# Kernel optimization log

Measured on AMD Instinct MI355X. Metric: run time of the kernel, lower is better.

The kernel has to match this reference:

```python
import jax, jax.numpy as jnp
import numpy as np

N_NODES = 100000
N_EDGES = 1600000
N_GRAPHS = 64
D_IN, D_HID, D_LAT = 2, 64, 32


def setup_inputs() -> dict:
    key = jax.random.key(0)
    k1, k2, k3, k4, k5, k6, k7 = jax.random.split(key, 7)
    x = jax.random.normal(k1, (N_NODES, D_IN), dtype=jnp.float32)
    edge_index = jax.random.randint(k2, (2, N_EDGES), 0, N_NODES, dtype=jnp.int64)
    batch = jnp.sort(jax.random.randint(k3, (N_NODES,), 0, N_GRAPHS, dtype=jnp.int64))
    # GCNConv params (glorot-ish scale)
    W1 = jax.random.normal(k4, (D_IN, D_HID), dtype=jnp.float32) * (1.0 / np.sqrt(D_IN))
    b1 = jnp.zeros((D_HID,), dtype=jnp.float32)
    W2 = jax.random.normal(k5, (D_HID, D_LAT), dtype=jnp.float32) * (1.0 / np.sqrt(D_HID))
    b2 = jnp.zeros((D_LAT,), dtype=jnp.float32)
    return {"x": x, "W1": W1, "b1": b1, "W2": W2, "b2": b2,
            "edge_index": edge_index, "batch": batch}


def _gcn_conv(x, W, b, src, dst, n_nodes):
    """PyG GCNConv: add self-loops, symmetric deg^-1/2 normalization, linear, scatter-add."""
    h = x @ W  # [N, d_out]
    loop = jnp.arange(n_nodes, dtype=src.dtype)
    src_f = jnp.concatenate([src, loop])
    dst_f = jnp.concatenate([dst, loop])
    deg = jax.ops.segment_sum(jnp.ones_like(dst_f, dtype=h.dtype), dst_f,
                              num_segments=n_nodes)  # in-degree incl. self-loop
    dis = jnp.where(deg > 0, jax.lax.rsqrt(deg), 0.0)
    norm = dis[src_f] * dis[dst_f]  # [E+N]
    msg = h[src_f] * norm[:, None]  # edge gather (memory-bound)
    out = jax.ops.segment_sum(msg, dst_f, num_segments=n_nodes)
    return out + b


def reference(x, W1, b1, W2, b2, edge_index, batch):
    src, dst = edge_index[0], edge_index[1]
    n = x.shape[0]
    h = jax.nn.relu(_gcn_conv(x, W1, b1, src, dst, n))
    z = _gcn_conv(h, W2, b2, src, dst, n)
    # global_mean_pool over graph ids
    sums = jax.ops.segment_sum(z, batch, num_segments=N_GRAPHS)
    cnts = jax.ops.segment_sum(jnp.ones((n,), dtype=z.dtype), batch,
                               num_segments=N_GRAPHS)
    return sums / jnp.maximum(cnts, 1.0)[:, None]
```

## Files before the change

kernel.cpp:

```cpp
#include <hip/hip_runtime.h>
#include <hip/hip_fp16.h>

#define N_NODES  100000
#define N_EDGES  1600000
#define N_GRAPHS 64
#define NBUCK    391
#define NBLK     256
#define CHUNK    (N_EDGES / NBLK)
#define NODEBLK  1563

#define OFF_GSTART 0
#define OFF_ROWPTR 128
#define OFF_DIS    100224
#define OFF_S      200320
#define OFF_CSR    400384
#define OFF_Q      2000384
#define OFF_BHIST  2000384
#define OFF_BOFFL  2100736
#define OFF_BSUM   2201088
#define OFF_BSTART 2201600
#define OFF_TMP    2202112

typedef float fvec2 __attribute__((ext_vector_type(2)));

__device__ __forceinline__ int excl_scan_256(int v, int* wsum) {
  int t = threadIdx.x, lane = t & 63, w = t >> 6;
  int x = v;
#pragma unroll
  for (int off = 1; off < 64; off <<= 1) {
    int y = __shfl_up(x, off, 64);
    if (lane >= off) x += y;
  }
  if (lane == 63) wsum[w] = x;
  __syncthreads();
  if (t == 0) {
    int r = 0;
#pragma unroll
    for (int i = 0; i < 4; ++i) { int tv = wsum[i]; wsum[i] = r; r += tv; }
  }
  __syncthreads();
  return x - v + wsum[w];
}

__device__ __forceinline__ int excl_scan_512(int v, int* wsum) {
  int t = threadIdx.x, lane = t & 63, w = t >> 6;
  int x = v;
#pragma unroll
  for (int off = 1; off < 64; off <<= 1) {
    int y = __shfl_up(x, off, 64);
    if (lane >= off) x += y;
  }
  if (lane == 63) wsum[w] = x;
  __syncthreads();
  if (t == 0) {
    int r = 0;
#pragma unroll
    for (int i = 0; i < 8; ++i) { int tv = wsum[i]; wsum[i] = r; r += tv; }
  }
  __syncthreads();
  return x - v + wsum[w];
}

__global__ void k_hist(const int* __restrict__ dst, int* __restrict__ bhist) {
  __shared__ int hist[NBUCK];
  int t = threadIdx.x, k = blockIdx.x;
  for (int b = t; b < NBUCK; b += 256) hist[b] = 0;
  __syncthreads();
  int e0 = k * CHUNK, e1 = e0 + CHUNK;
  for (int e = e0 + t; e < e1; e += 256) atomicAdd(&hist[dst[e] >> 8], 1);
  __syncthreads();
  for (int b = t; b < NBUCK; b += 256) bhist[b * NBLK + k] = hist[b];
}

__global__ void k_scan_a(const int* __restrict__ bhist, int* __restrict__ boffl,
                         int* __restrict__ bsum, const int* __restrict__ batch,
                         int* __restrict__ gstart) {
  __shared__ int wsum[4];
  int t = threadIdx.x, b = blockIdx.x;
  int i = b * 256 + t;
  if (i < N_NODES) {
    int bi = batch[i];
    if (i == 0) {
      for (int g = 0; g <= bi; ++g) gstart[g] = 0;
    } else {
      int bp = batch[i - 1];
      for (int g = bp + 1; g <= bi; ++g) gstart[g] = i;
    }
    if (i == N_NODES - 1) {
      for (int g = bi + 1; g <= N_GRAPHS; ++g) gstart[g] = N_NODES;
    }
  }
  int v = bhist[b * NBLK + t];
  int ex = excl_scan_256(v, wsum);
  boffl[b * NBLK + t] = ex;
  if (t == NBLK - 1) bsum[b] = ex + v;
}

__global__ void k_scan_b(const int* __restrict__ bsum, int* __restrict__ bstart,
                         float* __restrict__ pooled) {
  __shared__ int wsum[8];
  int t = threadIdx.x;
  for (int i = t; i < N_GRAPHS * 32; i += 512) pooled[i] = 0.f;
  int v = (t < NBUCK) ? bsum[t] : 0;
  int ex = excl_scan_512(v, wsum);
  if (t <= NBUCK) bstart[t] = ex;
}

__global__ void k_scatter(const int* __restrict__ src, const int* __restrict__ dst,
                          const int* __restrict__ bstart, const int* __restrict__ boffl,
                          int* __restrict__ tmp) {
  __shared__ int sbase[NBUCK];
  __shared__ int fill[NBUCK];
  int t = threadIdx.x, k = blockIdx.x;
  for (int b = t; b < NBUCK; b += 256) {
    sbase[b] = bstart[b] + boffl[b * NBLK + k];
    fill[b] = 0;
  }
  __syncthreads();
  int e0 = k * CHUNK, e1 = e0 + CHUNK;
  for (int e = e0 + t; e < e1; e += 256) {
    int s_ = src[e], d_ = dst[e];
    int b = d_ >> 8;
    int pos = sbase[b] + atomicAdd(&fill[b], 1);
    tmp[pos] = (s_ << 8) | (d_ & 255);
  }
}

__global__ void k_fine(const int* __restrict__ tmp, const int* __restrict__ bstart,
                       const float* __restrict__ x, int* __restrict__ csr_src,
                       int* __restrict__ row_ptr, float* __restrict__ dis,
                       float2* __restrict__ s) {
  __shared__ int hist[256];
  __shared__ int fill[256];
  __shared__ int wsum[4];
  int t = threadIdx.x, b = blockIdx.x;
  int base_n = b << 8;
  int e0 = bstart[b], e1 = bstart[b + 1];
  hist[t] = 0;
  __syncthreads();
  for (int e = e0 + t; e < e1; e += 256) atomicAdd(&hist[tmp[e] & 255], 1);
  __syncthreads();
  int h = hist[t];
  int ex = excl_scan_256(h, wsum);
  hist[t] = ex;
  fill[t] = 0;
  int nn = min(256, N_NODES - base_n);
  if (t < nn) {
    int v = base_n + t;
    row_ptr[v] = e0 + ex;
    float dv = rsqrtf((float)(h + 1));
    dis[v] = dv;
    float2 xv = ((const float2*)x)[v];
    s[v] = make_float2(xv.x * dv, xv.y * dv);
  }
  if (b == NBUCK - 1 && t == 0) row_ptr[N_NODES] = e1;
  __syncthreads();
  for (int e = e0 + t; e < e1; e += 256) {
    int p = tmp[e];
    int fine = p & 255;
    int pos = e0 + hist[fine] + atomicAdd(&fill[fine], 1);
    csr_src[pos] = p >> 8;
  }
}

__global__ void k_layer1(const float2* __restrict__ s, const float* __restrict__ dis,
                         const int* __restrict__ row_ptr, const int* __restrict__ csr_src,
                         const float* __restrict__ W1, const float* __restrict__ b1,
                         const float* __restrict__ W2, int4* __restrict__ q8) {
  __shared__ float4 sWB[64];
  __shared__ float4 sW2[512];
  int tid = threadIdx.x;
  if (tid < 64) sWB[tid] = make_float4(W1[tid], W1[64 + tid], b1[tid], 0.f);
  for (int i = tid; i < 512; i += 256) sW2[i] = ((const float4*)W2)[i];
  __syncthreads();
  int v = blockIdx.x * 256 + tid;
  if (v >= N_NODES) return;
  int beg = row_ptr[v], end = row_ptr[v + 1];
  float2 sv = s[v];
  float t0 = sv.x, t1 = sv.y;
  int k = beg;
  for (; k + 4 <= end; k += 4) {
    int u0 = csr_src[k], u1 = csr_src[k + 1], u2 = csr_src[k + 2], u3 = csr_src[k + 3];
    float2 a = s[u0], b = s[u1], c = s[u2], d = s[u3];
    t0 += (a.x + b.x) + (c.x + d.x);
    t1 += (a.y + b.y) + (c.y + d.y);
  }
  for (; k < end; ++k) {
    float2 su = s[csr_src[k]];
    t0 += su.x;
    t1 += su.y;
  }
  float dv = dis[v];
  t0 *= dv;
  t1 *= dv;
  float4 a4[8];
#pragma unroll
  for (int m = 0; m < 8; ++m) a4[m] = make_float4(0.f, 0.f, 0.f, 0.f);
  for (int j = 0; j < 64; ++j) {
    float4 wb = sWB[j];
    float r = fmaxf(fmaf(t0, wb.x, fmaf(t1, wb.y, wb.z)), 0.f);
#pragma unroll
    for (int m = 0; m < 8; ++m) {
      float4 w = sW2[j * 8 + m];
      a4[m].x = fmaf(r, w.x, a4[m].x);
      a4[m].y = fmaf(r, w.y, a4[m].y);
      a4[m].z = fmaf(r, w.z, a4[m].z);
      a4[m].w = fmaf(r, w.w, a4[m].w);
    }
  }
  int pk[8];
#pragma unroll
  for (int m = 0; m < 8; ++m) {
    int wrd = __builtin_amdgcn_cvt_pk_fp8_f32(a4[m].x * dv, a4[m].y * dv, 0, false);
    wrd = __builtin_amdgcn_cvt_pk_fp8_f32(a4[m].z * dv, a4[m].w * dv, wrd, true);
    pk[m] = wrd;
  }
  q8[v * 2]     = make_int4(pk[0], pk[1], pk[2], pk[3]);
  q8[v * 2 + 1] = make_int4(pk[4], pk[5], pk[6], pk[7]);
}

__device__ __forceinline__ float4 qdec(unsigned int d) {
  fvec2 lo = __builtin_amdgcn_cvt_pk_f32_fp8(d, false);
  fvec2 hi = __builtin_amdgcn_cvt_pk_f32_fp8(d, true);
  return make_float4(lo.x, lo.y, hi.x, hi.y);
}

__global__ void k_layer2(const unsigned int* __restrict__ q, const float* __restrict__ dis,
                         const int* __restrict__ row_ptr, const int* __restrict__ csr_src,
                         const int* __restrict__ batch, float* __restrict__ pooled) {
  __shared__ float4 red[32][9];
  int t = threadIdx.x;
  int fp = t & 7;
  int rg = t >> 3;
  int vb = blockIdx.x * 64;
  int nlast = min(vb + 63, N_NODES - 1);
  bool uniform = (batch[vb] == batch[nlast]);
  int v0 = vb + rg * 2;
  int v1 = min(v0 + 2, N_NODES);
  float4 acc = make_float4(0.f, 0.f, 0.f, 0.f);
  int curg = (v0 < N_NODES) ? batch[v0] : -1;
  for (int v = v0; v < v1; ++v) {
    if (!uniform) {
      int g = batch[v];
      if (g != curg) {
        int base = curg * 32 + fp * 4;
        atomicAdd(&pooled[base],     acc.x);
        atomicAdd(&pooled[base + 1], acc.y);
        atomicAdd(&pooled[base + 2], acc.z);
        atomicAdd(&pooled[base + 3], acc.w);
        acc = make_float4(0.f, 0.f, 0.f, 0.f);
        curg = g;
      }
    }
    int e0 = row_ptr[v], e1 = row_ptr[v + 1];
    float4 z = qdec(q[v * 8 + fp]);
    int k = e0;
    for (; k + 8 <= e1; k += 8) {
      int u0 = csr_src[k],     u1 = csr_src[k + 1], u2 = csr_src[k + 2], u3 = csr_src[k + 3];
      int u4 = csr_src[k + 4], u5 = csr_src[k + 5], u6 = csr_src[k + 6], u7 = csr_src[k + 7];
      float4 f0 = qdec(q[u0 * 8 + fp]);
      float4 f1 = qdec(q[u1 * 8 + fp]);
      float4 f2 = qdec(q[u2 * 8 + fp]);
      float4 f3 = qdec(q[u3 * 8 + fp]);
      float4 f4 = qdec(q[u4 * 8 + fp]);
      float4 f5 = qdec(q[u5 * 8 + fp]);
      float4 f6 = qdec(q[u6 * 8 + fp]);
      float4 f7 = qdec(q[u7 * 8 + fp]);
      z.x += ((f0.x + f1.x) + (f2.x + f3.x)) + ((f4.x + f5.x) + (f6.x + f7.x));
      z.y += ((f0.y + f1.y) + (f2.y + f3.y)) + ((f4.y + f5.y) + (f6.y + f7.y));
      z.z += ((f0.z + f1.z) + (f2.z + f3.z)) + ((f4.z + f5.z) + (f6.z + f7.z));
      z.w += ((f0.w + f1.w) + (f2.w + f3.w)) + ((f4.w + f5.w) + (f6.w + f7.w));
    }
    for (; k < e1; ++k) {
      float4 f = qdec(q[csr_src[k] * 8 + fp]);
      z.x += f.x; z.y += f.y; z.z += f.z; z.w += f.w;
    }
    float dvv = dis[v];
    acc.x = fmaf(z.x, dvv, acc.x);
    acc.y = fmaf(z.y, dvv, acc.y);
    acc.z = fmaf(z.z, dvv, acc.z);
    acc.w = fmaf(z.w, dvv, acc.w);
  }
  if (uniform) {
    red[rg][fp] = acc;
    __syncthreads();
    if (t < 8) {
      float4 ssum = make_float4(0.f, 0.f, 0.f, 0.f);
#pragma unroll
      for (int r = 0; r < 32; ++r) {
        float4 x4 = red[r][t];
        ssum.x += x4.x; ssum.y += x4.y; ssum.z += x4.z; ssum.w += x4.w;
      }
      int gg = batch[vb];
      int base = gg * 32 + t * 4;
      atomicAdd(&pooled[base],     ssum.x);
      atomicAdd(&pooled[base + 1], ssum.y);
      atomicAdd(&pooled[base + 2], ssum.z);
      atomicAdd(&pooled[base + 3], ssum.w);
    }
  } else if (v0 < N_NODES) {
    int base = curg * 32 + fp * 4;
    atomicAdd(&pooled[base],     acc.x);
    atomicAdd(&pooled[base + 1], acc.y);
    atomicAdd(&pooled[base + 2], acc.z);
    atomicAdd(&pooled[base + 3], acc.w);
  }
}

__global__ void k_final(float* __restrict__ out, const int* __restrict__ gstart,
                        const float* __restrict__ b2) {
  int i = blockIdx.x * 256 + threadIdx.x;
  if (i < N_GRAPHS * 32) {
    int g = i >> 5, l = i & 31;
    int c = gstart[g + 1] - gstart[g];
    out[i] = (c > 0) ? out[i] / (float)c + b2[l] : 0.f;
  }
}

extern "C" void kernel_launch(void* const* d_in, const int* in_sizes, int n_in,
                              void* d_out, int out_size, void* d_ws, size_t ws_size,
                              hipStream_t stream) {
  (void)in_sizes; (void)n_in; (void)out_size; (void)ws_size;
  const float* x   = (const float*)d_in[0];
  const float* W1  = (const float*)d_in[1];
  const float* b1  = (const float*)d_in[2];
  const float* W2  = (const float*)d_in[3];
  const float* b2  = (const float*)d_in[4];
  const int* edge  = (const int*)d_in[5];
  const int* batch = (const int*)d_in[6];
  const int* src = edge;
  const int* dst = edge + N_EDGES;
  float* out = (float*)d_out;

  int* ws      = (int*)d_ws;
  int* gstart  = ws + OFF_GSTART;
  int* row_ptr = ws + OFF_ROWPTR;
  float* dis   = (float*)(ws + OFF_DIS);
  float2* s    = (float2*)(ws + OFF_S);
  int* csr_src = ws + OFF_CSR;
  int4* q8     = (int4*)(ws + OFF_Q);
  int* bhist   = ws + OFF_BHIST;
  int* boffl   = ws + OFF_BOFFL;
  int* bsum    = ws + OFF_BSUM;
  int* bstart  = ws + OFF_BSTART;
  int* tmp     = ws + OFF_TMP;

  k_hist<<<NBLK, 256, 0, stream>>>(dst, bhist);
  k_scan_a<<<NBUCK, 256, 0, stream>>>(bhist, boffl, bsum, batch, gstart);
  k_scan_b<<<1, 512, 0, stream>>>(bsum, bstart, out);
  k_scatter<<<NBLK, 256, 0, stream>>>(src, dst, bstart, boffl, tmp);
  k_fine<<<NBUCK, 256, 0, stream>>>(tmp, bstart, x, csr_src, row_ptr, dis, s);
  k_layer1<<<(N_NODES + 255) / 256, 256, 0, stream>>>(s, dis, row_ptr, csr_src,
                                                      W1, b1, W2, q8);
  k_layer2<<<NODEBLK, 256, 0, stream>>>((const unsigned int*)q8, dis, row_ptr,
                                        csr_src, batch, out);
  k_final<<<8, 256, 0, stream>>>(out, gstart, b2);
}
```

Before: 97.16 us.

## Fuse scan and finalize kernels via last-block pattern; rework layer1 to two nodes per thread

```diff
diff --git a/kernel.cpp b/kernel.cpp
--- a/kernel.cpp
+++ b/kernel.cpp
@@ -10,6 +10,7 @@
 #define NODEBLK  1563
 
 #define OFF_GSTART 0
+#define OFF_CNT    80
 #define OFF_ROWPTR 128
 #define OFF_DIS    100224
 #define OFF_S      200320
@@ -42,28 +43,11 @@
   return x - v + wsum[w];
 }
 
-__device__ __forceinline__ int excl_scan_512(int v, int* wsum) {
-  int t = threadIdx.x, lane = t & 63, w = t >> 6;
-  int x = v;
-#pragma unroll
-  for (int off = 1; off < 64; off <<= 1) {
-    int y = __shfl_up(x, off, 64);
-    if (lane >= off) x += y;
-  }
-  if (lane == 63) wsum[w] = x;
-  __syncthreads();
-  if (t == 0) {
-    int r = 0;
-#pragma unroll
-    for (int i = 0; i < 8; ++i) { int tv = wsum[i]; wsum[i] = r; r += tv; }
-  }
-  __syncthreads();
-  return x - v + wsum[w];
-}
-
-__global__ void k_hist(const int* __restrict__ dst, int* __restrict__ bhist) {
+__global__ void k_hist(const int* __restrict__ dst, int* __restrict__ bhist,
+                       int* __restrict__ cnts) {
   __shared__ int hist[NBUCK];
   int t = threadIdx.x, k = blockIdx.x;
+  if (k == 0 && t == 0) { cnts[0] = 0; cnts[1] = 0; }
   for (int b = t; b < NBUCK; b += 256) hist[b] = 0;
   __syncthreads();
   int e0 = k * CHUNK, e1 = e0 + CHUNK;
@@ -74,8 +58,10 @@
 
 __global__ void k_scan_a(const int* __restrict__ bhist, int* __restrict__ boffl,
                          int* __restrict__ bsum, const int* __restrict__ batch,
-                         int* __restrict__ gstart) {
+                         int* __restrict__ gstart, int* __restrict__ bstart,
+                         float* __restrict__ pooled, int* __restrict__ cnts) {
   __shared__ int wsum[4];
+  __shared__ int lastflag;
   int t = threadIdx.x, b = blockIdx.x;
   int i = b * 256 + t;
   if (i < N_NODES) {
@@ -94,16 +80,21 @@
   int ex = excl_scan_256(v, wsum);
   boffl[b * NBLK + t] = ex;
   if (t == NBLK - 1) bsum[b] = ex + v;
-}
-
-__global__ void k_scan_b(const int* __restrict__ bsum, int* __restrict__ bstart,
-                         float* __restrict__ pooled) {
-  __shared__ int wsum[8];
-  int t = threadIdx.x;
-  for (int i = t; i < N_GRAPHS * 32; i += 512) pooled[i] = 0.f;
-  int v = (t < NBUCK) ? bsum[t] : 0;
-  int ex = excl_scan_512(v, wsum);
-  if (t <= NBUCK) bstart[t] = ex;
+  __threadfence();
+  if (t == 0) lastflag = (atomicAdd(&cnts[0], 1) == gridDim.x - 1) ? 1 : 0;
+  __syncthreads();
+  if (!lastflag) return;
+  __threadfence();
+  for (int j = t; j < N_GRAPHS * 32; j += 256) pooled[j] = 0.f;
+  int v0 = (t < NBUCK) ? bsum[t] : 0;
+  int ex0 = excl_scan_256(v0, wsum);
+  bstart[t] = ex0;
+  __syncthreads();
+  int tot0 = bstart[255] + ((255 < NBUCK) ? bsum[255] : 0);
+  int idx = 256 + t;
+  int v1 = (idx < NBUCK) ? bsum[idx] : 0;
+  int ex1 = excl_scan_256(v1, wsum);
+  if (idx <= NBUCK) bstart[idx] = tot0 + ex1;
 }
 
 __global__ void k_scatter(const int* __restrict__ src, const int* __restrict__ dst,
@@ -163,60 +154,97 @@
   }
 }
 
-__global__ void k_layer1(const float2* __restrict__ s, const float* __restrict__ dis,
-                         const int* __restrict__ row_ptr, const int* __restrict__ csr_src,
-                         const float* __restrict__ W1, const float* __restrict__ b1,
-                         const float* __restrict__ W2, int4* __restrict__ q8) {
+__global__ void __launch_bounds__(64)
+k_layer1(const float2* __restrict__ s, const int* __restrict__ row_ptr,
+         const int* __restrict__ csr_src, const float* __restrict__ W1,
+         const float* __restrict__ b1, const float* __restrict__ W2,
+         int4* __restrict__ q8) {
   __shared__ float4 sWB[64];
   __shared__ float4 sW2[512];
-  int tid = threadIdx.x;
-  if (tid < 64) sWB[tid] = make_float4(W1[tid], W1[64 + tid], b1[tid], 0.f);
-  for (int i = tid; i < 512; i += 256) sW2[i] = ((const float4*)W2)[i];
-  __syncthreads();
-  int v = blockIdx.x * 256 + tid;
-  if (v >= N_NODES) return;
-  int beg = row_ptr[v], end = row_ptr[v + 1];
-  float2 sv = s[v];
-  float t0 = sv.x, t1 = sv.y;
-  int k = beg;
-  for (; k + 4 <= end; k += 4) {
-    int u0 = csr_src[k], u1 = csr_src[k + 1], u2 = csr_src[k + 2], u3 = csr_src[k + 3];
-    float2 a = s[u0], b = s[u1], c = s[u2], d = s[u3];
-    t0 += (a.x + b.x) + (c.x + d.x);
-    t1 += (a.y + b.y) + (c.y + d.y);
-  }
-  for (; k < end; ++k) {
-    float2 su = s[csr_src[k]];
-    t0 += su.x;
-    t1 += su.y;
-  }
-  float dv = dis[v];
-  t0 *= dv;
-  t1 *= dv;
-  float4 a4[8];
-#pragma unroll
-  for (int m = 0; m < 8; ++m) a4[m] = make_float4(0.f, 0.f, 0.f, 0.f);
+  int t = threadIdx.x;
+  sWB[t] = make_float4(W1[t], W1[64 + t], b1[t], 0.f);
+#pragma unroll
+  for (int i = 0; i < 8; ++i) sW2[i * 64 + t] = ((const float4*)W2)[i * 64 + t];
+  __syncthreads();
+  int base = blockIdx.x * 128;
+  int vA = base + t, vB = base + 64 + t;
+  bool okA = vA < N_NODES, okB = vB < N_NODES;
+  float tA0 = 0.f, tA1 = 0.f, tB0 = 0.f, tB1 = 0.f, dA = 0.f, dB = 0.f;
+  if (okA) {
+    int beg = row_ptr[vA], end = row_ptr[vA + 1];
+    float2 sv = s[vA];
+    tA0 = sv.x; tA1 = sv.y;
+    int k = beg;
+    for (; k + 4 <= end; k += 4) {
+      float2 a = s[csr_src[k]], b = s[csr_src[k + 1]];
+      float2 c = s[csr_src[k + 2]], d = s[csr_src[k + 3]];
+      tA0 += (a.x + b.x) + (c.x + d.x);
+      tA1 += (a.y + b.y) + (c.y + d.y);
+    }
+    for (; k < end; ++k) { float2 su = s[csr_src[k]]; tA0 += su.x; tA1 += su.y; }
+    dA = rsqrtf((float)(end - beg + 1));
+    tA0 *= dA; tA1 *= dA;
+  }
+  if (okB) {
+    int beg = row_ptr[vB], end = row_ptr[vB + 1];
+    float2 sv = s[vB];
+    tB0 = sv.x; tB1 = sv.y;
+    int k = beg;
+    for (; k + 4 <= end; k += 4) {
+      float2 a = s[csr_src[k]], b = s[csr_src[k + 1]];
+      float2 c = s[csr_src[k + 2]], d = s[csr_src[k + 3]];
+      tB0 += (a.x + b.x) + (c.x + d.x);
+      tB1 += (a.y + b.y) + (c.y + d.y);
+    }
+    for (; k < end; ++k) { float2 su = s[csr_src[k]]; tB0 += su.x; tB1 += su.y; }
+    dB = rsqrtf((float)(end - beg + 1));
+    tB0 *= dB; tB1 *= dB;
+  }
+  float4 aA[8], aB[8];
+#pragma unroll
+  for (int m = 0; m < 8; ++m) {
+    aA[m] = make_float4(0.f, 0.f, 0.f, 0.f);
+    aB[m] = make_float4(0.f, 0.f, 0.f, 0.f);
+  }
   for (int j = 0; j < 64; ++j) {
     float4 wb = sWB[j];
-    float r = fmaxf(fmaf(t0, wb.x, fmaf(t1, wb.y, wb.z)), 0.f);
+    float rA = fmaxf(fmaf(tA0, wb.x, fmaf(tA1, wb.y, wb.z)), 0.f);
+    float rB = fmaxf(fmaf(tB0, wb.x, fmaf(tB1, wb.y, wb.z)), 0.f);
 #pragma unroll
     for (int m = 0; m < 8; ++m) {
       float4 w = sW2[j * 8 + m];
-      a4[m].x = fmaf(r, w.x, a4[m].x);
-      a4[m].y = fmaf(r, w.y, a4[m].y);
-      a4[m].z = fmaf(r, w.z, a4[m].z);
-      a4[m].w = fmaf(r, w.w, a4[m].w);
-    }
-  }
-  int pk[8];
-#pragma unroll
-  for (int m = 0; m < 8; ++m) {
-    int wrd = __builtin_amdgcn_cvt_pk_fp8_f32(a4[m].x * dv, a4[m].y * dv, 0, false);
-    wrd = __builtin_amdgcn_cvt_pk_fp8_f32(a4[m].z * dv, a4[m].w * dv, wrd, true);
-    pk[m] = wrd;
-  }
-  q8[v * 2]     = make_int4(pk[0], pk[1], pk[2], pk[3]);
-  q8[v * 2 + 1] = make_int4(pk[4], pk[5], pk[6], pk[7]);
+      aA[m].x = fmaf(rA, w.x, aA[m].x);
+      aA[m].y = fmaf(rA, w.y, aA[m].y);
+      aA[m].z = fmaf(rA, w.z, aA[m].z);
+      aA[m].w = fmaf(rA, w.w, aA[m].w);
+      aB[m].x = fmaf(rB, w.x, aB[m].x);
+      aB[m].y = fmaf(rB, w.y, aB[m].y);
+      aB[m].z = fmaf(rB, w.z, aB[m].z);
+      aB[m].w = fmaf(rB, w.w, aB[m].w);
+    }
+  }
+  if (okA) {
+    int pk[8];
+#pragma unroll
+    for (int m = 0; m < 8; ++m) {
+      int wrd = __builtin_amdgcn_cvt_pk_fp8_f32(aA[m].x * dA, aA[m].y * dA, 0, false);
+      wrd = __builtin_amdgcn_cvt_pk_fp8_f32(aA[m].z * dA, aA[m].w * dA, wrd, true);
+      pk[m] = wrd;
+    }
+    q8[vA * 2]     = make_int4(pk[0], pk[1], pk[2], pk[3]);
+    q8[vA * 2 + 1] = make_int4(pk[4], pk[5], pk[6], pk[7]);
+  }
+  if (okB) {
+    int pk[8];
+#pragma unroll
+    for (int m = 0; m < 8; ++m) {
+      int wrd = __builtin_amdgcn_cvt_pk_fp8_f32(aB[m].x * dB, aB[m].y * dB, 0, false);
+      wrd = __builtin_amdgcn_cvt_pk_fp8_f32(aB[m].z * dB, aB[m].w * dB, wrd, true);
+      pk[m] = wrd;
+    }
+    q8[vB * 2]     = make_int4(pk[0], pk[1], pk[2], pk[3]);
+    q8[vB * 2 + 1] = make_int4(pk[4], pk[5], pk[6], pk[7]);
+  }
 }
 
 __device__ __forceinline__ float4 qdec(unsigned int d) {
@@ -227,8 +255,11 @@
 
 __global__ void k_layer2(const unsigned int* __restrict__ q, const float* __restrict__ dis,
                          const int* __restrict__ row_ptr, const int* __restrict__ csr_src,
-                         const int* __restrict__ batch, float* __restrict__ pooled) {
+                         const int* __restrict__ batch, float* __restrict__ pooled,
+                         const int* __restrict__ gstart, const float* __restrict__ b2,
+                         int* __restrict__ cnts) {
   __shared__ float4 red[32][9];
+  __shared__ int lastflag;
   int t = threadIdx.x;
   int fp = t & 7;
   int rg = t >> 3;
@@ -305,15 +336,16 @@
     atomicAdd(&pooled[base + 2], acc.z);
     atomicAdd(&pooled[base + 3], acc.w);
   }
-}
-
-__global__ void k_final(float* __restrict__ out, const int* __restrict__ gstart,
-                        const float* __restrict__ b2) {
-  int i = blockIdx.x * 256 + threadIdx.x;
-  if (i < N_GRAPHS * 32) {
+  __threadfence();
+  if (t == 0) lastflag = (atomicAdd(&cnts[1], 1) == gridDim.x - 1) ? 1 : 0;
+  __syncthreads();
+  if (!lastflag) return;
+  __threadfence();
+  for (int i = t; i < N_GRAPHS * 32; i += 256) {
     int g = i >> 5, l = i & 31;
     int c = gstart[g + 1] - gstart[g];
-    out[i] = (c > 0) ? out[i] / (float)c + b2[l] : 0.f;
+    float val = pooled[i];
+    pooled[i] = (c > 0) ? val / (float)c + b2[l] : 0.f;
   }
 }
 
@@ -334,6 +366,7 @@
 
   int* ws      = (int*)d_ws;
   int* gstart  = ws + OFF_GSTART;
+  int* cnts    = ws + OFF_CNT;
   int* row_ptr = ws + OFF_ROWPTR;
   float* dis   = (float*)(ws + OFF_DIS);
   float2* s    = (float2*)(ws + OFF_S);
@@ -345,14 +378,13 @@
   int* bstart  = ws + OFF_BSTART;
   int* tmp     = ws + OFF_TMP;
 
-  k_hist<<<NBLK, 256, 0, stream>>>(dst, bhist);
-  k_scan_a<<<NBUCK, 256, 0, stream>>>(bhist, boffl, bsum, batch, gstart);
-  k_scan_b<<<1, 512, 0, stream>>>(bsum, bstart, out);
+  k_hist<<<NBLK, 256, 0, stream>>>(dst, bhist, cnts);
+  k_scan_a<<<NBUCK, 256, 0, stream>>>(bhist, boffl, bsum, batch, gstart,
+                                      bstart, out, cnts);
   k_scatter<<<NBLK, 256, 0, stream>>>(src, dst, bstart, boffl, tmp);
   k_fine<<<NBUCK, 256, 0, stream>>>(tmp, bstart, x, csr_src, row_ptr, dis, s);
-  k_layer1<<<(N_NODES + 255) / 256, 256, 0, stream>>>(s, dis, row_ptr, csr_src,
-                                                      W1, b1, W2, q8);
+  k_layer1<<<(N_NODES + 127) / 128, 64, 0, stream>>>(s, row_ptr, csr_src,
+                                                     W1, b1, W2, q8);
   k_layer2<<<NODEBLK, 256, 0, stream>>>((const unsigned int*)q8, dis, row_ptr,
-                                        csr_src, batch, out);
-  k_final<<<8, 256, 0, stream>>>(out, gstart, b2);
-}
+                                        csr_src, batch, out, gstart, b2, cnts);
+}
```

New measurement: 217.4 us. 124% more time.
